# Kernel optimization log

Hardware: AMD Instinct MI355X
Metric: run time of the kernel (lower is better)

The kernel has to match this reference:

```python
import jax, jax.numpy as jnp
import numpy as np

FS = 16000.0
SOUND_SPEED = 343.0
MAX_ORDER = 10
FILTER_LEN = 81            # fractional-delay sinc filter taps (torchaudio default)
PAD = FILTER_LEN // 2      # 40
RIR_LEN = 8000             # static RIR length; bounds max delay for 10 m rooms, order 10

# ---- static image-source lattice: all (i,j,k) with |i|+|j|+|k| <= MAX_ORDER ----
_ind = np.arange(-MAX_ORDER, MAX_ORDER + 1)
_g = np.stack(np.meshgrid(_ind, _ind, _ind, indexing="ij"), -1).reshape(-1, 3)
_g = _g[np.abs(_g).sum(-1) <= MAX_ORDER]                      # (n_img=1561, 3)
XYZ = jnp.asarray(_g, dtype=jnp.float32)                      # (n_img, 3)
EXP_LO = jnp.asarray(np.abs(np.floor(_g / 2.0)), jnp.float32)        # reflections off x=0/y=0/z=0 walls
EXP_HI = jnp.asarray(np.abs(np.floor((_g + 1) / 2.0)), jnp.float32)  # reflections off far walls
ODD = jnp.asarray(_g % 2 == 1)                                # (n_img, 3) bool


def _hann(x, T):
    # truncated Hann window used by the fractional-delay filter
    return jnp.where(jnp.abs(x) <= T / 2, 0.5 * (1.0 + jnp.cos(2.0 * jnp.pi * x / T)), 0.0)


def _rir_one(room, mic, src, absorption):
    # room, mic, src: (3,) metres; absorption: (6,) per-wall absorption coeff
    # image-source positions: mirror source across walls per parity of lattice index
    img = jnp.where(ODD, room * (XYZ + 1.0) - src, room * XYZ + src)   # (n_img, 3)
    tr = jnp.sqrt(1.0 - absorption)                                     # wall reflection coeffs (6,)
    att = jnp.prod((tr[::2] ** EXP_LO) * (tr[1::2] ** EXP_HI), axis=-1)  # (n_img,)
    dist = jnp.linalg.norm(img - mic, axis=-1)                           # (n_img,)
    amp = att / dist                                                     # 1/r spreading
    delay = dist * FS / SOUND_SPEED                                      # delay in samples (float)
    delay_i = jnp.ceil(delay)                                            # integer anchor
    n = jnp.arange(-PAD, PAD + 1, dtype=jnp.float32)                     # (81,)
    x = n[None, :] + delay_i[:, None] - delay[:, None]                   # (n_img, 81)
    irs = amp[:, None] * jnp.sinc(x) * _hann(x, 2 * PAD)                 # windowed-sinc frac delay
    # scatter-add each 81-tap filter at offset delay_i - PAD into the RIR buffer
    idx = delay_i.astype(jnp.int32)[:, None] - PAD + jnp.arange(FILTER_LEN, dtype=jnp.int32)
    valid = (idx >= 0) & (idx < RIR_LEN)
    rir = jnp.zeros((RIR_LEN,), irs.dtype).at[jnp.clip(idx, 0, RIR_LEN - 1)].add(
        jnp.where(valid, irs, 0.0))
    return rir


def setup_inputs() -> dict:
    key = jax.random.key(0)
    k1, k2, k3, k4 = jax.random.split(key, 4)
    B = 256
    room = 3.0 + 7.0 * jax.random.uniform(k1, (B, 3), jnp.float32)       # room dims in [3,10] m
    mic_f = 0.05 + 0.40 * jax.random.uniform(k2, (B, 3), jnp.float32)    # mic frac in [0.05,0.45]
    src_f = 0.55 + 0.40 * jax.random.uniform(k3, (B, 3), jnp.float32)    # src frac in [0.55,0.95]
    absorp = 0.1 + 0.4 * jax.random.uniform(k4, (B, 1), jnp.float32)     # absorption in [0.1,0.5]
    inp = jnp.concatenate([room, mic_f, src_f, absorp], axis=1)          # (B, 10)
    return {"input": inp}


def reference(input):
    room = input[:, 0:3]
    mic = input[:, 3:6] * room
    src = input[:, 6:9] * room
    absorption = jnp.repeat(input[:, 9:10], 6, axis=1)                   # uniform over 6 walls
    rir = jax.vmap(_rir_one)(room, mic, src, absorption)                 # (B, RIR_LEN)
    dist = jnp.linalg.norm(mic - src, axis=1)
    toa = 40.0 + FS * dist / SOUND_SPEED                                 # (B,)
    return rir, toa
```

## Files before the change

kernel.cpp:

```cpp
#include <hip/hip_runtime.h>
#include <math.h>

#define NB 256
#define NIMG 1561
#define RIRLEN 8000
#define PADI 40
#define NTHREADS 1024
#define NWAVES (NTHREADS / 64)
#define NBKT 505
#define NSTARTP 512
#define NPAIR 63

struct ImgTab { unsigned int v[NIMG]; };

constexpr ImgTab build_tab() {
    ImgTab t{};
    int n = 0;
    for (int x = -10; x <= 10; ++x)
        for (int y = -10; y <= 10; ++y)
            for (int z = -10; z <= 10; ++z) {
                int ax = x < 0 ? -x : x;
                int ay = y < 0 ? -y : y;
                int az = z < 0 ? -z : z;
                int l1 = ax + ay + az;
                if (l1 <= 10) {
                    t.v[n++] = (unsigned)(x + 10) | ((unsigned)(y + 10) << 5) |
                               ((unsigned)(z + 10) << 10) | ((unsigned)l1 << 15);
                }
            }
    return t;
}

constexpr int tab_count() {
    int n = 0;
    for (int x = -10; x <= 10; ++x)
        for (int y = -10; y <= 10; ++y)
            for (int z = -10; z <= 10; ++z) {
                int ax = x < 0 ? -x : x;
                int ay = y < 0 ? -y : y;
                int az = z < 0 ? -z : z;
                if (ax + ay + az <= 10) ++n;
            }
    return n;
}
static_assert(tab_count() == NIMG, "image count mismatch");

__constant__ ImgTab c_tab = build_tab();

__global__ __launch_bounds__(NTHREADS) void
rir_kernel(const float* __restrict__ in, float* __restrict__ out) {
    __shared__ float4 s_rec[NIMG + 1];
    __shared__ float  s_trpow[11];
    __shared__ int    s_hist[NSTARTP];
    __shared__ int    s_start[NSTARTP];
    __shared__ int    s_cursor[NBKT];
    __shared__ int    s_qnext;
    __shared__ int    s_nspike;
    __shared__ int    s_spike_idx[64];
    __shared__ float  s_spike_amp[64];

    const int b    = blockIdx.x >> 1;
    const int half = blockIdx.x & 1;
    const int tid  = threadIdx.x;
    const float* p = in + b * 10;

    const int qlo = half ? 32 : 0;
    const int qhi = half ? NPAIR : 32;

    if (tid < NSTARTP) s_hist[tid] = 0;
    if (tid == 0) {
        float tr = sqrtf(1.0f - p[9]);
        float pw = 1.0f;
        for (int k = 0; k <= 10; ++k) { s_trpow[k] = pw; pw *= tr; }
        s_nspike = 0;
        s_qnext  = qlo + NWAVES;
        s_rec[NIMG] = make_float4(0.0f, 0.0f, 0.0f, -1.0e6f);
    }
    __syncthreads();

    const float rx = p[0], ry = p[1], rz = p[2];
    const float mx = p[3] * rx, my = p[4] * ry, mz = p[5] * rz;
    const float sx = p[6] * rx, sy = p[7] * ry, sz = p[8] * rz;
    const float K = 16000.0f / 343.0f;
    const float INV_PI = 0.31830988618379067154f;

    float4 rec[2];
    int ibkt[2]  = {0, 0};
    bool ivalid[2] = {false, false};

    for (int u = 0; u < 2; ++u) {
        int i = tid + u * NTHREADS;
        if (i < NIMG) {
            unsigned v = c_tab.v[i];
            int gx = (int)(v & 31u) - 10;
            int gy = (int)((v >> 5) & 31u) - 10;
            int gz = (int)((v >> 10) & 31u) - 10;
            int l1 = (int)(v >> 15);

            float ix = (gx & 1) ? rx * (float)(gx + 1) - sx : rx * (float)gx + sx;
            float iy = (gy & 1) ? ry * (float)(gy + 1) - sy : ry * (float)gy + sy;
            float iz = (gz & 1) ? rz * (float)(gz + 1) - sz : rz * (float)gz + sz;

            float dx = ix - mx, dy = iy - my, dz = iz - mz;
            float dist = sqrtf(dx * dx + dy * dy + dz * dz);

            float amp  = s_trpow[l1] / dist;
            float d    = dist * K;
            float dlc  = ceilf(d);
            float frac = dlc - d;
            int   idlc = (int)dlc;
            int   base = idlc - PADI;

            if (base < RIRLEN) {
                if (frac == 0.0f) {
                    if (idlc < RIRLEN) {
                        int sp = atomicAdd(&s_nspike, 1);
                        if (sp < 64) { s_spike_idx[sp] = idlc; s_spike_amp[sp] = amp; }
                    }
                } else {
                    float spf = (frac < 1.0e-3f) ? frac : (sinpif(frac) * INV_PI);
                    float S   = amp * spf;
                    if (idlc & 1) S = -S;
                    float hS  = 0.5f * S;
                    float cd  = cospif(d * 0.025f);
                    float sd  = sinpif(d * 0.025f);
                    rec[u] = make_float4(hS, hS * cd, hS * sd, d);
                    ibkt[u]   = (base + 80) >> 4;
                    ivalid[u] = true;
                    atomicAdd(&s_hist[ibkt[u]], 1);
                }
            }
        }
    }
    __syncthreads();

    if (tid < 64) {
        int base_i = tid * 8;
        int v[8], pre[8];
        int run = 0;
#pragma unroll
        for (int j = 0; j < 8; ++j) {
            v[j] = s_hist[base_i + j];
            pre[j] = run;
            run += v[j];
        }
        int t = run;
#pragma unroll
        for (int d2 = 1; d2 < 64; d2 <<= 1) {
            int y = __shfl_up(t, d2);
            if (tid >= d2) t += y;
        }
        int excl = t - run;
#pragma unroll
        for (int j = 0; j < 8; ++j) {
            int idx = base_i + j;
            int sv  = excl + pre[j];
            s_start[idx] = sv;
            if (idx < NBKT) s_cursor[idx] = sv;
        }
    }
    __syncthreads();

    for (int u = 0; u < 2; ++u) {
        if (ivalid[u]) {
            int pos = atomicAdd(&s_cursor[ibkt[u]], 1);
            s_rec[pos] = rec[u];
        }
    }
    __syncthreads();

    const int wave = tid >> 6;
    const int lane = tid & 63;
    const int h    = lane >> 5;
    const int l5   = lane & 31;
    const float sgn  = (l5 & 1) ? -1.0f : 1.0f;
    const float vinf = __builtin_inff();
    const float c32  = -0.80901699437494742410f;
    const float s32  =  0.58778525229247312917f;
    float* __restrict__ ob = out + (size_t)b * RIRLEN;

    int q = qlo + wave;
    while (q < qhi) {
        const int n0 = (q << 7) + (h << 6) + l5;
        const int n1 = n0 + 32;
        const float fn0 = (float)n0;
        const float cn0 = cospif(fn0 * 0.025f), sn0 = sinpif(fn0 * 0.025f);
        const float cnn1 = cn0 * c32 - sn0 * s32;
        const float snn1 = sn0 * c32 + cn0 * s32;

        const int loA = s_start[8 * q];
        const int hiA = s_start[8 * q + 9];
        const int loB = s_start[8 * q + 4];
        const int hiB = s_start[8 * q + 13];
        const int lenA = hiA - loA, lenB = hiB - loB;
        const int lmin = (lenA < lenB) ? lenA : lenB;
        const int lmax = (lenA > lenB) ? lenA : lenB;
        const int lo   = h ? loB : loA;
        const int hi   = h ? hiB : hiA;

        float acc0 = 0.0f, acc1 = 0.0f;
#pragma clang loop unroll_count(8)
        for (int it = 0; it < lmin; ++it) {
            float4 r = s_rec[lo + it];
            float x0 = fn0 - r.w;
            float x1 = x0 + 32.0f;
            float xm0 = (fabsf(x0) < 40.0f) ? x0 : vinf;
            float xm1 = (fabsf(x1) < 40.0f) ? x1 : vinf;
            float t0 = fmaf(r.y, cn0, r.x);  t0 = fmaf(r.z, sn0, t0);
            float t1 = fmaf(r.y, cnn1, r.x); t1 = fmaf(r.z, snn1, t1);
            acc0 = fmaf(t0, __builtin_amdgcn_rcpf(xm0), acc0);
            acc1 = fmaf(t1, __builtin_amdgcn_rcpf(xm1), acc1);
        }
        for (int it = lmin; it < lmax; ++it) {
            int k = lo + it;
            float4 r = s_rec[(k < hi) ? k : NIMG];
            float x0 = fn0 - r.w;
            float x1 = x0 + 32.0f;
            float xm0 = (fabsf(x0) < 40.0f) ? x0 : vinf;
            float xm1 = (fabsf(x1) < 40.0f) ? x1 : vinf;
            float t0 = fmaf(r.y, cn0, r.x);  t0 = fmaf(r.z, sn0, t0);
            float t1 = fmaf(r.y, cnn1, r.x); t1 = fmaf(r.z, snn1, t1);
            acc0 = fmaf(t0, __builtin_amdgcn_rcpf(xm0), acc0);
            acc1 = fmaf(t1, __builtin_amdgcn_rcpf(xm1), acc1);
        }
        if (n0 < RIRLEN) ob[n0] = acc0 * sgn;
        if (n1 < RIRLEN) ob[n1] = acc1 * sgn;

        int nq;
        if (lane == 0) nq = atomicAdd(&s_qnext, 1);
        q = __shfl(nq, 0);
    }

    __syncthreads();
    int nsp = s_nspike; nsp = (nsp < 64) ? nsp : 64;
    if (tid < nsp) {
        int idx = s_spike_idx[tid];
        int rlo = half ? 4096 : 0;
        int rhi = half ? RIRLEN : 4096;
        if (idx >= rlo && idx < rhi) atomicAdd(&ob[idx], s_spike_amp[tid]);
    }

    if (tid == 0 && half == 0) {
        float dx = mx - sx, dy = my - sy, dz = mz - sz;
        out[(size_t)NB * RIRLEN + b] = 40.0f + sqrtf(dx * dx + dy * dy + dz * dz) * K;
    }
}

extern "C" void kernel_launch(void* const* d_in, const int* in_sizes, int n_in,
                              void* d_out, int out_size, void* d_ws, size_t ws_size,
                              hipStream_t stream) {
    const float* in = (const float*)d_in[0];
    float* out = (float*)d_out;
    rir_kernel<<<dim3(NB * 2), dim3(NTHREADS), 0, stream>>>(in, out);
}
```

Baseline: 89.29 us.

## Merge block halves into one block per batch and share one reciprocal per tap pair

```diff
diff --git a/kernel.cpp b/kernel.cpp
--- a/kernel.cpp
+++ b/kernel.cpp
@@ -59,13 +59,9 @@
     __shared__ int    s_spike_idx[64];
     __shared__ float  s_spike_amp[64];
 
-    const int b    = blockIdx.x >> 1;
-    const int half = blockIdx.x & 1;
-    const int tid  = threadIdx.x;
+    const int b   = blockIdx.x;
+    const int tid = threadIdx.x;
     const float* p = in + b * 10;
-
-    const int qlo = half ? 32 : 0;
-    const int qhi = half ? NPAIR : 32;
 
     if (tid < NSTARTP) s_hist[tid] = 0;
     if (tid == 0) {
@@ -73,7 +69,7 @@
         float pw = 1.0f;
         for (int k = 0; k <= 10; ++k) { s_trpow[k] = pw; pw *= tr; }
         s_nspike = 0;
-        s_qnext  = qlo + NWAVES;
+        s_qnext  = NWAVES;
         s_rec[NIMG] = make_float4(0.0f, 0.0f, 0.0f, -1.0e6f);
     }
     __syncthreads();
@@ -104,7 +100,7 @@
             float dx = ix - mx, dy = iy - my, dz = iz - mz;
             float dist = sqrtf(dx * dx + dy * dy + dz * dz);
 
-            float amp  = s_trpow[l1] / dist;
+            float amp  = s_trpow[l1] * __builtin_amdgcn_rcpf(dist);
             float d    = dist * K;
             float dlc  = ceilf(d);
             float frac = dlc - d;
@@ -173,14 +169,13 @@
     const int lane = tid & 63;
     const int h    = lane >> 5;
     const int l5   = lane & 31;
-    const float sgn  = (l5 & 1) ? -1.0f : 1.0f;
-    const float vinf = __builtin_inff();
-    const float c32  = -0.80901699437494742410f;
-    const float s32  =  0.58778525229247312917f;
+    const float sgn = (l5 & 1) ? -1.0f : 1.0f;
+    const float c32 = -0.80901699437494742410f;
+    const float s32 =  0.58778525229247312917f;
     float* __restrict__ ob = out + (size_t)b * RIRLEN;
 
-    int q = qlo + wave;
-    while (q < qhi) {
+    int q = wave;
+    while (q < NPAIR) {
         const int n0 = (q << 7) + (h << 6) + l5;
         const int n1 = n0 + 32;
         const float fn0 = (float)n0;
@@ -204,24 +199,26 @@
             float4 r = s_rec[lo + it];
             float x0 = fn0 - r.w;
             float x1 = x0 + 32.0f;
-            float xm0 = (fabsf(x0) < 40.0f) ? x0 : vinf;
-            float xm1 = (fabsf(x1) < 40.0f) ? x1 : vinf;
+            float pr = __builtin_amdgcn_rcpf(x0 * x1);
             float t0 = fmaf(r.y, cn0, r.x);  t0 = fmaf(r.z, sn0, t0);
             float t1 = fmaf(r.y, cnn1, r.x); t1 = fmaf(r.z, snn1, t1);
-            acc0 = fmaf(t0, __builtin_amdgcn_rcpf(xm0), acc0);
-            acc1 = fmaf(t1, __builtin_amdgcn_rcpf(xm1), acc1);
+            t0 = (fabsf(x0) < 40.0f) ? t0 : 0.0f;
+            t1 = (fabsf(x1) < 40.0f) ? t1 : 0.0f;
+            acc0 = fmaf(t0 * x1, pr, acc0);
+            acc1 = fmaf(t1 * x0, pr, acc1);
         }
         for (int it = lmin; it < lmax; ++it) {
             int k = lo + it;
             float4 r = s_rec[(k < hi) ? k : NIMG];
             float x0 = fn0 - r.w;
             float x1 = x0 + 32.0f;
-            float xm0 = (fabsf(x0) < 40.0f) ? x0 : vinf;
-            float xm1 = (fabsf(x1) < 40.0f) ? x1 : vinf;
+            float pr = __builtin_amdgcn_rcpf(x0 * x1);
             float t0 = fmaf(r.y, cn0, r.x);  t0 = fmaf(r.z, sn0, t0);
             float t1 = fmaf(r.y, cnn1, r.x); t1 = fmaf(r.z, snn1, t1);
-            acc0 = fmaf(t0, __builtin_amdgcn_rcpf(xm0), acc0);
-            acc1 = fmaf(t1, __builtin_amdgcn_rcpf(xm1), acc1);
+            t0 = (fabsf(x0) < 40.0f) ? t0 : 0.0f;
+            t1 = (fabsf(x1) < 40.0f) ? t1 : 0.0f;
+            acc0 = fmaf(t0 * x1, pr, acc0);
+            acc1 = fmaf(t1 * x0, pr, acc1);
         }
         if (n0 < RIRLEN) ob[n0] = acc0 * sgn;
         if (n1 < RIRLEN) ob[n1] = acc1 * sgn;
@@ -233,14 +230,9 @@
 
     __syncthreads();
     int nsp = s_nspike; nsp = (nsp < 64) ? nsp : 64;
-    if (tid < nsp) {
-        int idx = s_spike_idx[tid];
-        int rlo = half ? 4096 : 0;
-        int rhi = half ? RIRLEN : 4096;
-        if (idx >= rlo && idx < rhi) atomicAdd(&ob[idx], s_spike_amp[tid]);
-    }
-
-    if (tid == 0 && half == 0) {
+    if (tid < nsp) atomicAdd(&ob[s_spike_idx[tid]], s_spike_amp[tid]);
+
+    if (tid == 0) {
         float dx = mx - sx, dy = my - sy, dz = mz - sz;
         out[(size_t)NB * RIRLEN + b] = 40.0f + sqrtf(dx * dx + dy * dy + dz * dz) * K;
     }
@@ -251,5 +243,5 @@
                               hipStream_t stream) {
     const float* in = (const float*)d_in[0];
     float* out = (float*)d_out;
-    rir_kernel<<<dim3(NB * 2), dim3(NTHREADS), 0, stream>>>(in, out);
-}
+    rir_kernel<<<dim3(NB), dim3(NTHREADS), 0, stream>>>(in, out);
+}
```

New measurement: 78.98 us. 1.13x faster.
